# Kernel tuning notes

Hardware: AMD Instinct MI355X
Metric: run time of the kernel (lower is better)

## Reference

```python
import jax, jax.numpy as jnp
import numpy as np

B = 16384
S = 7          # grid cells per side
C = 30         # 2 boxes * 5 + 20 classes
GX = 7.0       # num_gridx = labels.shape[-2]
GY = 30.0      # num_gridy = labels.shape[-1]  (faithful to the original code's size()[-2:] bug)


def setup_inputs() -> dict:
    key = jax.random.key(0)
    k1, k2, k3 = jax.random.split(key, 3)
    # keep w,h away from 0 so sqrt grads are finite
    pred = jax.random.uniform(k1, (B, S, S, C), dtype=jnp.float32, minval=0.05, maxval=0.95)
    labels = jax.random.uniform(k2, (B, S, S, C), dtype=jnp.float32, minval=0.05, maxval=0.95)
    obj = jax.random.bernoulli(k3, 0.3, (B, S, S)).astype(jnp.float32)
    labels = labels.at[..., 4].set(obj)
    return {"pred": pred, "labels": labels}


def _boxes_xyxy(t, off, mg, ng):
    # t[..., off:off+4] = (x, y, w, h) relative to cell; convert to xyxy
    cx = (t[..., off] + mg) / GX
    cy = (t[..., off + 1] + ng) / GY
    w = t[..., off + 2]
    h = t[..., off + 3]
    return jnp.stack([cx - w / 2, cy - h / 2, cx + w / 2, cy + h / 2], axis=-1)


def _iou(b1, b2):
    ix1 = jnp.maximum(b1[..., 0], b2[..., 0])
    iy1 = jnp.maximum(b1[..., 1], b2[..., 1])
    ix2 = jnp.minimum(b1[..., 2], b2[..., 2])
    iy2 = jnp.minimum(b1[..., 3], b2[..., 3])
    iw = jnp.maximum(ix2 - ix1, 0.0)
    ih = jnp.maximum(iy2 - iy1, 0.0)
    inter = iw * ih
    a1 = (b1[..., 2] - b1[..., 0]) * (b1[..., 3] - b1[..., 1])
    a2 = (b2[..., 2] - b2[..., 0]) * (b2[..., 3] - b2[..., 1])
    union = a1 + a2 - inter
    pos = inter > 0
    return jnp.where(pos, inter / jnp.where(pos, union, 1.0), 0.0)


def reference(pred, labels):
    n_batch = pred.shape[0]
    # grid offsets: m indexes axis 1, n indexes axis 2
    mg = jnp.arange(S, dtype=pred.dtype)[:, None]   # (7,1)
    ng = jnp.arange(S, dtype=pred.dtype)[None, :]   # (1,7)

    pb1 = _boxes_xyxy(pred, 0, mg, ng)
    pb2 = _boxes_xyxy(pred, 5, mg, ng)
    gb = _boxes_xyxy(labels, 0, mg, ng)
    iou1 = _iou(pb1, gb)   # (B,7,7)
    iou2 = _iou(pb2, gb)
    sel1 = iou1 >= iou2
    obj = labels[..., 4] == 1.0

    coor1 = (jnp.sum((pred[..., 0:2] - labels[..., 0:2]) ** 2, -1)
             + jnp.sum((jnp.sqrt(pred[..., 2:4]) - jnp.sqrt(labels[..., 2:4])) ** 2, -1))
    coor2 = (jnp.sum((pred[..., 5:7] - labels[..., 5:7]) ** 2, -1)
             + jnp.sum((jnp.sqrt(pred[..., 7:9]) - jnp.sqrt(labels[..., 7:9])) ** 2, -1))
    coor = 5.0 * jnp.where(sel1, coor1, coor2)

    d1 = (pred[..., 4] - iou1) ** 2
    d2 = (pred[..., 9] - iou2) ** 2
    obj_confi = jnp.where(sel1, d1, d2)
    noobj_at_obj = 0.5 * jnp.where(sel1, d2, d1)

    class_loss = jnp.sum((pred[..., 10:] - labels[..., 10:]) ** 2, -1)

    noobj_at_noobj = 0.5 * (pred[..., 4] ** 2 + pred[..., 9] ** 2)

    per_cell = jnp.where(obj, coor + obj_confi + noobj_at_obj + class_loss, noobj_at_noobj)
    return jnp.sum(per_cell) / n_batch
```

## Files before the change

### kernel.cpp

```cpp
#include <hip/hip_runtime.h>


#define NCELLS (16384 * 49)
#define INV_NB (1.0f / 16384.0f)
#define CPB 64
#define NBLK (NCELLS / CPB)
#define SLAB_F4 (CPB * 30 / 4)
#define SLAB_F (CPB * 30)

__device__ __forceinline__ float iou_xyxy(float ax1, float ay1, float ax2, float ay2,
                                          float bx1, float by1, float bx2, float by2) {
    float ix1 = fmaxf(ax1, bx1);
    float iy1 = fmaxf(ay1, by1);
    float ix2 = fminf(ax2, bx2);
    float iy2 = fminf(ay2, by2);
    float iw = fmaxf(ix2 - ix1, 0.0f);
    float ih = fmaxf(iy2 - iy1, 0.0f);
    float inter = iw * ih;
    float a1 = (ax2 - ax1) * (ay2 - ay1);
    float a2 = (bx2 - bx1) * (by2 - by1);
    float uni = a1 + a2 - inter;
    return (inter > 0.0f) ? (inter / uni) : 0.0f;
}

__global__ __launch_bounds__(64, 2) void yolo_loss_stage1(const float* __restrict__ pred,
                                                          const float* __restrict__ labels,
                                                          float* __restrict__ partials) {
    __shared__ float sm[2 * SLAB_F];

    const int t = threadIdx.x;
    const int b = blockIdx.x;

    const float4* gp4 = reinterpret_cast<const float4*>(pred) + (size_t)b * SLAB_F4;
    const float4* gl4 = reinterpret_cast<const float4*>(labels) + (size_t)b * SLAB_F4;

    float4 r[15];
#pragma unroll
    for (int i = 0; i < 15; ++i) {
        int idx = i * 64 + t;
        r[i] = (idx < SLAB_F4) ? gp4[idx] : gl4[idx - SLAB_F4];
    }
    float4* sm4 = reinterpret_cast<float4*>(sm);
#pragma unroll
    for (int i = 0; i < 15; ++i) {
        sm4[i * 64 + t] = r[i];
    }
    __syncthreads();

    const int gcell = b * CPB + t;
    const int rem = gcell % 49;
    const float fm = (float)(rem / 7);
    const float fn = (float)(rem % 7);

    const float2* ps = reinterpret_cast<const float2*>(sm + t * 30);
    const float2* ls = reinterpret_cast<const float2*>(sm + SLAB_F + t * 30);

    float pv[30], lv[30];
#pragma unroll
    for (int k = 0; k < 15; ++k) {
        float2 a = ps[k];
        pv[2 * k] = a.x; pv[2 * k + 1] = a.y;
    }
#pragma unroll
    for (int k = 0; k < 15; ++k) {
        float2 bb = ls[k];
        lv[2 * k] = bb.x; lv[2 * k + 1] = bb.y;
    }

    float cx = (pv[0] + fm) / 7.0f;
    float cy = (pv[1] + fn) / 30.0f;
    float w = pv[2], h = pv[3];
    float p1x1 = cx - w * 0.5f, p1y1 = cy - h * 0.5f;
    float p1x2 = cx + w * 0.5f, p1y2 = cy + h * 0.5f;

    cx = (pv[5] + fm) / 7.0f;
    cy = (pv[6] + fn) / 30.0f;
    w = pv[7]; h = pv[8];
    float p2x1 = cx - w * 0.5f, p2y1 = cy - h * 0.5f;
    float p2x2 = cx + w * 0.5f, p2y2 = cy + h * 0.5f;

    cx = (lv[0] + fm) / 7.0f;
    cy = (lv[1] + fn) / 30.0f;
    w = lv[2]; h = lv[3];
    float gx1 = cx - w * 0.5f, gy1 = cy - h * 0.5f;
    float gx2 = cx + w * 0.5f, gy2 = cy + h * 0.5f;

    float iou1 = iou_xyxy(p1x1, p1y1, p1x2, p1y2, gx1, gy1, gx2, gy2);
    float iou2 = iou_xyxy(p2x1, p2y1, p2x2, p2y2, gx1, gy1, gx2, gy2);

    bool sel1 = (iou1 >= iou2);
    bool obj = (lv[4] == 1.0f);

    float dx = pv[0] - lv[0], dy = pv[1] - lv[1];
    float dw = sqrtf(pv[2]) - sqrtf(lv[2]);
    float dh = sqrtf(pv[3]) - sqrtf(lv[3]);
    float coor1 = dx * dx + dy * dy + dw * dw + dh * dh;

    dx = pv[5] - lv[5]; dy = pv[6] - lv[6];
    dw = sqrtf(pv[7]) - sqrtf(lv[7]);
    dh = sqrtf(pv[8]) - sqrtf(lv[8]);
    float coor2 = dx * dx + dy * dy + dw * dw + dh * dh;

    float coor = 5.0f * (sel1 ? coor1 : coor2);

    float d1 = pv[4] - iou1; d1 *= d1;
    float d2 = pv[9] - iou2; d2 *= d2;
    float obj_confi = sel1 ? d1 : d2;
    float noobj_at_obj = 0.5f * (sel1 ? d2 : d1);

    float cls = 0.0f;
#pragma unroll
    for (int k = 10; k < 30; ++k) {
        float d = pv[k] - lv[k];
        cls += d * d;
    }

    float noobj_at_noobj = 0.5f * (pv[4] * pv[4] + pv[9] * pv[9]);

    float per = obj ? (coor + obj_confi + noobj_at_obj + cls) : noobj_at_noobj;

    float acc = per;
#pragma unroll
    for (int off = 32; off > 0; off >>= 1) acc += __shfl_down(acc, off, 64);
    if (t == 0) partials[b] = acc;
}

__global__ __launch_bounds__(256) void yolo_loss_stage2(const float* __restrict__ partials,
                                                        float* __restrict__ out) {
    const int t = threadIdx.x;
    float acc = 0.0f;
#pragma unroll
    for (int i = 0; i < NBLK / 256; ++i) {
        acc += partials[i * 256 + t];
    }
#pragma unroll
    for (int off = 32; off > 0; off >>= 1) acc += __shfl_down(acc, off, 64);

    __shared__ float sbuf[4];
    if ((t & 63) == 0) sbuf[t >> 6] = acc;
    __syncthreads();
    if (t == 0) out[0] = (sbuf[0] + sbuf[1] + sbuf[2] + sbuf[3]) * INV_NB;
}

extern "C" void kernel_launch(void* const* d_in, const int* in_sizes, int n_in,
                              void* d_out, int out_size, void* d_ws, size_t ws_size,
                              hipStream_t stream) {
    const float* pred = (const float*)d_in[0];
    const float* labels = (const float*)d_in[1];
    float* out = (float*)d_out;
    float* partials = (float*)d_ws;

    yolo_loss_stage1<<<NBLK, 64, 0, stream>>>(pred, labels, partials);
    yolo_loss_stage2<<<1, 256, 0, stream>>>(partials, out);
}
```

Baseline: 203.2 us.

## Make stage1 persistent with register prefetch of the next slab

Stage1 now runs a fixed grid of 2560 blocks. Each block walks the 64-cell slabs in a grid-stride loop and issues the global float4 loads for the next slab into registers while it computes the current one from LDS. Per-thread sums accumulate across slabs, so stage2 reduces far fewer partials. The block-level __syncthreads is gone, which relies on a block being a single wave64; the smaller grid lowers concurrent waves per CU and depends on the prefetch to hide memory latency.

```diff
diff --git a/kernel.cpp b/kernel.cpp
--- a/kernel.cpp
+++ b/kernel.cpp
@@ -2,11 +2,12 @@
 
 
 #define NCELLS (16384 * 49)
+#define CPS 64
+#define NSLABS (NCELLS / CPS)
+#define GRID 2560
+#define SLAB_F (CPS * 30)
+#define SLAB_F4 (SLAB_F / 4)
 #define INV_NB (1.0f / 16384.0f)
-#define CPB 64
-#define NBLK (NCELLS / CPB)
-#define SLAB_F4 (CPB * 30 / 4)
-#define SLAB_F (CPB * 30)
 
 __device__ __forceinline__ float iou_xyxy(float ax1, float ay1, float ax2, float ay2,
                                           float bx1, float by1, float bx2, float by2) {
@@ -23,114 +24,130 @@
     return (inter > 0.0f) ? (inter / uni) : 0.0f;
 }
 
-__global__ __launch_bounds__(64, 2) void yolo_loss_stage1(const float* __restrict__ pred,
-                                                          const float* __restrict__ labels,
-                                                          float* __restrict__ partials) {
+__global__ __launch_bounds__(64, 3) void yolo_stage1(const float* __restrict__ pred,
+                                                     const float* __restrict__ labels,
+                                                     float* __restrict__ partials) {
     __shared__ float sm[2 * SLAB_F];
+    const int t = threadIdx.x;
 
-    const int t = threadIdx.x;
-    const int b = blockIdx.x;
+    float4 r0, r1, r2, r3, r4, r5, r6, r7, r8, r9, r10, r11, r12, r13, r14;
 
-    const float4* gp4 = reinterpret_cast<const float4*>(pred) + (size_t)b * SLAB_F4;
-    const float4* gl4 = reinterpret_cast<const float4*>(labels) + (size_t)b * SLAB_F4;
-
-    float4 r[15];
-#pragma unroll
-    for (int i = 0; i < 15; ++i) {
-        int idx = i * 64 + t;
-        r[i] = (idx < SLAB_F4) ? gp4[idx] : gl4[idx - SLAB_F4];
-    }
-    float4* sm4 = reinterpret_cast<float4*>(sm);
-#pragma unroll
-    for (int i = 0; i < 15; ++i) {
-        sm4[i * 64 + t] = r[i];
-    }
-    __syncthreads();
-
-    const int gcell = b * CPB + t;
-    const int rem = gcell % 49;
-    const float fm = (float)(rem / 7);
-    const float fn = (float)(rem % 7);
-
-    const float2* ps = reinterpret_cast<const float2*>(sm + t * 30);
-    const float2* ls = reinterpret_cast<const float2*>(sm + SLAB_F + t * 30);
-
-    float pv[30], lv[30];
-#pragma unroll
-    for (int k = 0; k < 15; ++k) {
-        float2 a = ps[k];
-        pv[2 * k] = a.x; pv[2 * k + 1] = a.y;
-    }
-#pragma unroll
-    for (int k = 0; k < 15; ++k) {
-        float2 bb = ls[k];
-        lv[2 * k] = bb.x; lv[2 * k + 1] = bb.y;
+#define ISSUE(s)                                                                  \
+    {                                                                             \
+        const float4* p4 = reinterpret_cast<const float4*>(pred) + (size_t)(s)*SLAB_F4;   \
+        const float4* l4 = reinterpret_cast<const float4*>(labels) + (size_t)(s)*SLAB_F4; \
+        r0 = p4[0 * 64 + t];  r1 = p4[1 * 64 + t];  r2 = p4[2 * 64 + t];          \
+        r3 = p4[3 * 64 + t];  r4 = p4[4 * 64 + t];  r5 = p4[5 * 64 + t];          \
+        r6 = p4[6 * 64 + t];                                                      \
+        r7 = (t < 32) ? p4[7 * 64 + t] : l4[7 * 64 + t - SLAB_F4];                \
+        r8 = l4[8 * 64 + t - SLAB_F4];   r9 = l4[9 * 64 + t - SLAB_F4];           \
+        r10 = l4[10 * 64 + t - SLAB_F4]; r11 = l4[11 * 64 + t - SLAB_F4];         \
+        r12 = l4[12 * 64 + t - SLAB_F4]; r13 = l4[13 * 64 + t - SLAB_F4];         \
+        r14 = l4[14 * 64 + t - SLAB_F4];                                          \
     }
 
-    float cx = (pv[0] + fm) / 7.0f;
-    float cy = (pv[1] + fn) / 30.0f;
-    float w = pv[2], h = pv[3];
-    float p1x1 = cx - w * 0.5f, p1y1 = cy - h * 0.5f;
-    float p1x2 = cx + w * 0.5f, p1y2 = cy + h * 0.5f;
+    float accthr = 0.0f;
+    int s = blockIdx.x;
+    ISSUE(s);
 
-    cx = (pv[5] + fm) / 7.0f;
-    cy = (pv[6] + fn) / 30.0f;
-    w = pv[7]; h = pv[8];
-    float p2x1 = cx - w * 0.5f, p2y1 = cy - h * 0.5f;
-    float p2x2 = cx + w * 0.5f, p2y2 = cy + h * 0.5f;
+    while (s < NSLABS) {
+        float4* sm4 = reinterpret_cast<float4*>(sm);
+        sm4[0 * 64 + t] = r0;   sm4[1 * 64 + t] = r1;   sm4[2 * 64 + t] = r2;
+        sm4[3 * 64 + t] = r3;   sm4[4 * 64 + t] = r4;   sm4[5 * 64 + t] = r5;
+        sm4[6 * 64 + t] = r6;   sm4[7 * 64 + t] = r7;   sm4[8 * 64 + t] = r8;
+        sm4[9 * 64 + t] = r9;   sm4[10 * 64 + t] = r10; sm4[11 * 64 + t] = r11;
+        sm4[12 * 64 + t] = r12; sm4[13 * 64 + t] = r13; sm4[14 * 64 + t] = r14;
 
-    cx = (lv[0] + fm) / 7.0f;
-    cy = (lv[1] + fn) / 30.0f;
-    w = lv[2]; h = lv[3];
-    float gx1 = cx - w * 0.5f, gy1 = cy - h * 0.5f;
-    float gx2 = cx + w * 0.5f, gy2 = cy + h * 0.5f;
+        const int snext = s + GRID;
+        if (snext < NSLABS) ISSUE(snext);
 
-    float iou1 = iou_xyxy(p1x1, p1y1, p1x2, p1y2, gx1, gy1, gx2, gy2);
-    float iou2 = iou_xyxy(p2x1, p2y1, p2x2, p2y2, gx1, gy1, gx2, gy2);
+        const int gcell = s * CPS + t;
+        const int rem = gcell % 49;
+        const float fm = (float)(rem / 7);
+        const float fn = (float)(rem % 7);
 
-    bool sel1 = (iou1 >= iou2);
-    bool obj = (lv[4] == 1.0f);
+        const float2* ps = reinterpret_cast<const float2*>(sm + t * 30);
+        const float2* ls = reinterpret_cast<const float2*>(sm + SLAB_F + t * 30);
 
-    float dx = pv[0] - lv[0], dy = pv[1] - lv[1];
-    float dw = sqrtf(pv[2]) - sqrtf(lv[2]);
-    float dh = sqrtf(pv[3]) - sqrtf(lv[3]);
-    float coor1 = dx * dx + dy * dy + dw * dw + dh * dh;
+        float pv[30], lv[30];
+#pragma unroll
+        for (int k = 0; k < 15; ++k) {
+            float2 a = ps[k];
+            pv[2 * k] = a.x; pv[2 * k + 1] = a.y;
+        }
+#pragma unroll
+        for (int k = 0; k < 15; ++k) {
+            float2 bb = ls[k];
+            lv[2 * k] = bb.x; lv[2 * k + 1] = bb.y;
+        }
 
-    dx = pv[5] - lv[5]; dy = pv[6] - lv[6];
-    dw = sqrtf(pv[7]) - sqrtf(lv[7]);
-    dh = sqrtf(pv[8]) - sqrtf(lv[8]);
-    float coor2 = dx * dx + dy * dy + dw * dw + dh * dh;
+        float cx = (pv[0] + fm) / 7.0f;
+        float cy = (pv[1] + fn) / 30.0f;
+        float w = pv[2], h = pv[3];
+        float p1x1 = cx - w * 0.5f, p1y1 = cy - h * 0.5f;
+        float p1x2 = cx + w * 0.5f, p1y2 = cy + h * 0.5f;
 
-    float coor = 5.0f * (sel1 ? coor1 : coor2);
+        cx = (pv[5] + fm) / 7.0f;
+        cy = (pv[6] + fn) / 30.0f;
+        w = pv[7]; h = pv[8];
+        float p2x1 = cx - w * 0.5f, p2y1 = cy - h * 0.5f;
+        float p2x2 = cx + w * 0.5f, p2y2 = cy + h * 0.5f;
 
-    float d1 = pv[4] - iou1; d1 *= d1;
-    float d2 = pv[9] - iou2; d2 *= d2;
-    float obj_confi = sel1 ? d1 : d2;
-    float noobj_at_obj = 0.5f * (sel1 ? d2 : d1);
+        cx = (lv[0] + fm) / 7.0f;
+        cy = (lv[1] + fn) / 30.0f;
+        w = lv[2]; h = lv[3];
+        float gx1 = cx - w * 0.5f, gy1 = cy - h * 0.5f;
+        float gx2 = cx + w * 0.5f, gy2 = cy + h * 0.5f;
 
-    float cls = 0.0f;
+        float iou1 = iou_xyxy(p1x1, p1y1, p1x2, p1y2, gx1, gy1, gx2, gy2);
+        float iou2 = iou_xyxy(p2x1, p2y1, p2x2, p2y2, gx1, gy1, gx2, gy2);
+
+        bool sel1 = (iou1 >= iou2);
+        bool obj = (lv[4] == 1.0f);
+
+        float dx = pv[0] - lv[0], dy = pv[1] - lv[1];
+        float dw = sqrtf(pv[2]) - sqrtf(lv[2]);
+        float dh = sqrtf(pv[3]) - sqrtf(lv[3]);
+        float coor1 = dx * dx + dy * dy + dw * dw + dh * dh;
+
+        dx = pv[5] - lv[5]; dy = pv[6] - lv[6];
+        dw = sqrtf(pv[7]) - sqrtf(lv[7]);
+        dh = sqrtf(pv[8]) - sqrtf(lv[8]);
+        float coor2 = dx * dx + dy * dy + dw * dw + dh * dh;
+
+        float coor = 5.0f * (sel1 ? coor1 : coor2);
+
+        float d1 = pv[4] - iou1; d1 *= d1;
+        float d2 = pv[9] - iou2; d2 *= d2;
+        float obj_confi = sel1 ? d1 : d2;
+        float noobj_at_obj = 0.5f * (sel1 ? d2 : d1);
+
+        float cls = 0.0f;
 #pragma unroll
-    for (int k = 10; k < 30; ++k) {
-        float d = pv[k] - lv[k];
-        cls += d * d;
+        for (int k = 10; k < 30; ++k) {
+            float d = pv[k] - lv[k];
+            cls += d * d;
+        }
+
+        float noobj_at_noobj = 0.5f * (pv[4] * pv[4] + pv[9] * pv[9]);
+
+        accthr += obj ? (coor + obj_confi + noobj_at_obj + cls) : noobj_at_noobj;
+
+        s = snext;
     }
 
-    float noobj_at_noobj = 0.5f * (pv[4] * pv[4] + pv[9] * pv[9]);
-
-    float per = obj ? (coor + obj_confi + noobj_at_obj + cls) : noobj_at_noobj;
-
-    float acc = per;
 #pragma unroll
-    for (int off = 32; off > 0; off >>= 1) acc += __shfl_down(acc, off, 64);
-    if (t == 0) partials[b] = acc;
+    for (int off = 32; off > 0; off >>= 1) accthr += __shfl_down(accthr, off, 64);
+    if (t == 0) partials[blockIdx.x] = accthr;
+#undef ISSUE
 }
 
-__global__ __launch_bounds__(256) void yolo_loss_stage2(const float* __restrict__ partials,
-                                                        float* __restrict__ out) {
+__global__ __launch_bounds__(256) void yolo_stage2(const float* __restrict__ partials,
+                                                   float* __restrict__ out) {
     const int t = threadIdx.x;
     float acc = 0.0f;
 #pragma unroll
-    for (int i = 0; i < NBLK / 256; ++i) {
+    for (int i = 0; i < GRID / 256; ++i) {
         acc += partials[i * 256 + t];
     }
 #pragma unroll
@@ -150,6 +167,6 @@
     float* out = (float*)d_out;
     float* partials = (float*)d_ws;
 
-    yolo_loss_stage1<<<NBLK, 64, 0, stream>>>(pred, labels, partials);
-    yolo_loss_stage2<<<1, 256, 0, stream>>>(partials, out);
+    yolo_stage1<<<GRID, 64, 0, stream>>>(pred, labels, partials);
+    yolo_stage2<<<1, 256, 0, stream>>>(partials, out);
 }
```

New measurement: 204.9 us. About the same (+0.8%).
